# Kernel optimization log

Measured on AMD Instinct MI355X. Metric: run time of the kernel, lower is better.

The kernel has to match this reference:

```python
import jax, jax.numpy as jnp
import numpy as np

EMBED_DIM = 1024
NUM_HEADS = 16
WINDOW = 128  # one-sided window length w; total span 2w+1


def setup_inputs() -> dict:
    key = jax.random.key(0)
    ks = jax.random.split(key, 9)
    D = EMBED_DIM
    x = jax.random.normal(ks[0], (2, 8192, D), dtype=jnp.float32)
    s = 0.02
    Wq = jax.random.normal(ks[1], (D, D), dtype=jnp.float32) * s
    bq = jax.random.normal(ks[2], (D,), dtype=jnp.float32) * s
    Wk = jax.random.normal(ks[3], (D, D), dtype=jnp.float32) * s
    bk = jax.random.normal(ks[4], (D,), dtype=jnp.float32) * s
    Wv = jax.random.normal(ks[5], (D, D), dtype=jnp.float32) * s
    bv = jax.random.normal(ks[6], (D,), dtype=jnp.float32) * s
    Wo = jax.random.normal(ks[7], (D, D), dtype=jnp.float32) * s
    bo = jax.random.normal(ks[8], (D,), dtype=jnp.float32) * s
    return {"x": x, "Wq": Wq, "bq": bq, "Wk": Wk, "bk": bk,
            "Wv": Wv, "bv": bv, "Wo": Wo, "bo": bo}


def _sliding_window_attention(x, Wq, bq, Wk, bk, Wv, bv, Wo, bo):
    B, S, D = x.shape
    H, w = NUM_HEADS, WINDOW
    hd = D // H
    bs = w            # block size = window_length; 3 blocks cover [i-w, i+w]
    nb = S // bs

    def proj(W, b):
        y = x @ W.T + b                              # torch Linear: x @ W.T + b
        return y.reshape(B, S, H, hd).transpose(0, 2, 1, 3)  # [B,H,S,hd]

    q = proj(Wq, bq)
    k = proj(Wk, bk)
    v = proj(Wv, bv)

    qb = q.reshape(B, H, nb, bs, hd)
    # pad K/V with one zero block on each side, then build 3-block contexts
    pad = ((0, 0), (0, 0), (bs, bs), (0, 0))
    kp = jnp.pad(k, pad).reshape(B, H, nb + 2, bs, hd)
    vp = jnp.pad(v, pad).reshape(B, H, nb + 2, bs, hd)
    k_ctx = jnp.concatenate([kp[:, :, :-2], kp[:, :, 1:-1], kp[:, :, 2:]], axis=3)  # [B,H,nb,3bs,hd]
    v_ctx = jnp.concatenate([vp[:, :, :-2], vp[:, :, 1:-1], vp[:, :, 2:]], axis=3)

    scale = 1.0 / np.sqrt(hd).astype(np.float32)
    scores = jnp.einsum('bhnqd,bhnkd->bhnqk', qb, k_ctx) * scale  # [B,H,nb,bs,3bs]

    # band mask: |k_pos - q_pos| <= w, and k_pos in [0, S)
    q_off = jnp.arange(bs)
    k_off = jnp.arange(3 * bs)
    rel = k_off[None, :] - bs - q_off[:, None]                # [bs,3bs]
    win_ok = jnp.abs(rel) <= w
    k_pos = (jnp.arange(nb)[:, None, None] - 1) * bs + k_off[None, None, :]
    valid = (k_pos >= 0) & (k_pos < S)                        # [nb,1,3bs]
    mask = win_ok[None] & valid                               # [nb,bs,3bs]

    scores = jnp.where(mask[None, None], scores, jnp.float32(-jnp.inf))
    weights = jax.nn.softmax(scores, axis=-1)

    out = jnp.einsum('bhnqk,bhnkd->bhnqd', weights, v_ctx)    # [B,H,nb,bs,hd]
    out = out.reshape(B, H, S, hd).transpose(0, 2, 1, 3).reshape(B, S, D)
    return out @ Wo.T + bo


def reference(x, Wq, bq, Wk, bk, Wv, bv, Wo, bo):
    return _sliding_window_attention(x, Wq, bq, Wk, bk, Wv, bv, Wo, bo)
```

## Files before the change

### kernel.cpp

```cpp
#include <hip/hip_runtime.h>

typedef __attribute__((ext_vector_type(4))) float f32x4;
typedef __attribute__((ext_vector_type(8))) short s16x8;

#define MFMA16(a, b, c) __builtin_amdgcn_mfma_f32_16x16x32_bf16((a), (b), (c), 0, 0, 0)

__device__ __forceinline__ unsigned short f2bf_bits(float f) {
  unsigned int u = __float_as_uint(f);
  unsigned int r = (u + 0x7fffu + ((u >> 16) & 1u)) >> 16;
  return (unsigned short)r;
}

__device__ __forceinline__ void gl_lds16(const void* g, void* l) {
  __builtin_amdgcn_global_load_lds((const __attribute__((address_space(1))) void*)g,
                                   (__attribute__((address_space(3))) void*)l, 16, 0, 0);
}

__global__ __launch_bounds__(256) void f2bf_kernel(const float* __restrict__ in,
                                                   unsigned short* __restrict__ out, int n4) {
  int idx = blockIdx.x * 256 + threadIdx.x;
  int stride = gridDim.x * 256;
  for (int i = idx; i < n4; i += stride) {
    float4 v = ((const float4*)in)[i];
    ushort4 o;
    o.x = f2bf_bits(v.x); o.y = f2bf_bits(v.y);
    o.z = f2bf_bits(v.z); o.w = f2bf_bits(v.w);
    ((ushort4*)out)[i] = o;
  }
}

__global__ __launch_bounds__(256) void f2bf_w4(const float* __restrict__ w0,
                                               const float* __restrict__ w1,
                                               const float* __restrict__ w2,
                                               const float* __restrict__ w3,
                                               unsigned short* __restrict__ o0,
                                               unsigned short* __restrict__ o1,
                                               unsigned short* __restrict__ o2,
                                               unsigned short* __restrict__ o3) {
  const int s = blockIdx.y;
  const float* in = (s == 0) ? w0 : (s == 1) ? w1 : (s == 2) ? w2 : w3;
  unsigned short* out = (s == 0) ? o0 : (s == 1) ? o1 : (s == 2) ? o2 : o3;
  int i = blockIdx.x * 256 + threadIdx.x;
  float4 v = ((const float4*)in)[i];
  ushort4 o;
  o.x = f2bf_bits(v.x); o.y = f2bf_bits(v.y);
  o.z = f2bf_bits(v.z); o.w = f2bf_bits(v.w);
  ((ushort4*)out)[i] = o;
}

#define GEMM_CORE64(A_, B_, K_)                                                       \
  f32x4 acc[4][4];                                                                    \
  _Pragma("unroll") for (int i = 0; i < 4; ++i)                                       \
      _Pragma("unroll") for (int j = 0; j < 4; ++j)                                   \
          acc[i][j] = (f32x4){0.f, 0.f, 0.f, 0.f};                                    \
  {                                                                                   \
    const int rb = tid >> 3;                                                          \
    const int cb = (((tid & 7) ^ (rb & 7))) * 8;                                      \
    _Pragma("unroll 1") for (int k0 = 0; k0 < (K_); k0 += 64) {                       \
      _Pragma("unroll") for (int i = 0; i < 4; ++i) {                                 \
        gl_lds16((A_) + (size_t)(rb + 32 * i) * (K_) + k0 + cb, &Al[(tid + 256 * i) * 8]); \
        gl_lds16((B_) + (size_t)(rb + 32 * i) * (K_) + k0 + cb, &Bl[(tid + 256 * i) * 8]); \
      }                                                                               \
      __syncthreads();                                                                \
      _Pragma("unroll") for (int ks = 0; ks < 2; ++ks) {                              \
        s16x8 af[4], bfr[4];                                                          \
        const int pch = ((ks * 4 + quad) ^ (l15 & 7)) * 8;                            \
        _Pragma("unroll") for (int i = 0; i < 4; ++i)                                 \
            af[i] = *(const s16x8*)&Al[(wm + i * 16 + l15) * 64 + pch];               \
        _Pragma("unroll") for (int j = 0; j < 4; ++j)                                 \
            bfr[j] = *(const s16x8*)&Bl[(wn + j * 16 + l15) * 64 + pch];              \
        _Pragma("unroll") for (int i = 0; i < 4; ++i)                                 \
            _Pragma("unroll") for (int j = 0; j < 4; ++j)                             \
                acc[i][j] = MFMA16(af[i], bfr[j], acc[i][j]);                         \
      }                                                                               \
      __syncthreads();                                                                \
    }                                                                                 \
  }

__global__ __launch_bounds__(256) void gemm_qkv(const unsigned short* __restrict__ A,
                                                const unsigned short* __restrict__ Wq,
                                                const unsigned short* __restrict__ Wk,
                                                const unsigned short* __restrict__ Wv,
                                                const float* __restrict__ bq,
                                                const float* __restrict__ bk,
                                                const float* __restrict__ bv,
                                                unsigned short* __restrict__ Qo,
                                                unsigned short* __restrict__ Ko,
                                                unsigned short* __restrict__ Vt) {
  __shared__ unsigned short Al[128 * 64];
  __shared__ unsigned short Bl[128 * 64];
  const int tid = threadIdx.x;
  const int lane = tid & 63, wave = tid >> 6;
  const int l15 = lane & 15, quad = lane >> 4;
  const int wm = (wave >> 1) * 64, wn = (wave & 1) * 64;
  const int bx = blockIdx.x;
  const int sel = blockIdx.y >> 3;
  const int by = blockIdx.y & 7;
  const int K = 1024, N = 1024;

  const unsigned short* W = (sel == 0) ? Wq : (sel == 1) ? Wk : Wv;
  const float* bias = (sel == 0) ? bq : (sel == 1) ? bk : bv;

  const unsigned short* Abase = A + (size_t)bx * 128 * K;
  const unsigned short* Bbase = W + (size_t)by * 128 * K;

  GEMM_CORE64(Abase, Bbase, K)

#pragma unroll
  for (int j = 0; j < 4; ++j) {
    const int cn = by * 128 + wn + j * 16 + l15;
    const float bj = bias[cn];
#pragma unroll
    for (int i = 0; i < 4; ++i) {
      const int r0 = bx * 128 + wm + i * 16 + quad * 4;
#pragma unroll
      for (int r = 0; r < 4; ++r) {
        const int row = r0 + r;
        const float v = acc[i][j][r] + bj;
        if (sel == 0) {
          Qo[(size_t)row * N + cn] = f2bf_bits(v);
        } else if (sel == 1) {
          Ko[(size_t)row * N + cn] = f2bf_bits(v);
        } else {
          Vt[((size_t)(row >> 13) * 1024 + cn) * 8192 + (row & 8191)] = f2bf_bits(v);
        }
      }
    }
  }
}

__global__ __launch_bounds__(256) void gemm_out(const unsigned short* __restrict__ A,
                                                const unsigned short* __restrict__ B,
                                                const float* __restrict__ bias,
                                                float* __restrict__ Cf) {
  __shared__ unsigned short Al[128 * 64];
  __shared__ unsigned short Bl[128 * 64];
  const int tid = threadIdx.x;
  const int lane = tid & 63, wave = tid >> 6;
  const int l15 = lane & 15, quad = lane >> 4;
  const int wm = (wave >> 1) * 64, wn = (wave & 1) * 64;
  const int bx = blockIdx.x, by = blockIdx.y;
  const int K = 1024, N = 1024;

  const unsigned short* Abase = A + (size_t)bx * 128 * K;
  const unsigned short* Bbase = B + (size_t)by * 128 * K;

  GEMM_CORE64(Abase, Bbase, K)

#pragma unroll
  for (int j = 0; j < 4; ++j) {
    const int cn = by * 128 + wn + j * 16 + l15;
    const float bj = bias[cn];
#pragma unroll
    for (int i = 0; i < 4; ++i) {
      const int r0 = bx * 128 + wm + i * 16 + quad * 4;
#pragma unroll
      for (int r = 0; r < 4; ++r) Cf[(size_t)(r0 + r) * N + cn] = acc[i][j][r] + bj;
    }
  }
}

__global__ __launch_bounds__(256, 3) void attn_kernel(const unsigned short* __restrict__ Q,
                                                      const unsigned short* __restrict__ Km,
                                                      const unsigned short* __restrict__ Vt,
                                                      unsigned short* __restrict__ O) {
  const int n = blockIdx.x;
  const int bh = blockIdx.y;
  const int b = bh >> 4, h = bh & 15;
  const int tid = threadIdx.x, lane = tid & 63, wave = tid >> 6;
  const int l15 = lane & 15, quad = lane >> 4;

  __shared__ unsigned short Kl[384 * 64];
  __shared__ unsigned short Ps[4][16 * 40];

  const int base_row = n * 128 - 128;

  for (int i = 0; i < 12; ++i) {
    const int c = i * 256 + tid;
    const int row = c >> 3;
    const int qc = (c & 7) ^ (row & 7);
    int gr = base_row + row;
    gr = min(max(gr, 0), 8191);
    gl_lds16(Km + (size_t)(b * 8192 + gr) * 1024 + h * 64 + qc * 8, &Kl[c * 8]);
  }
  __syncthreads();

  const unsigned short* Vbase = Vt + (size_t)bh * 64 * 8192;
  unsigned short* strip = &Ps[wave][0];

  for (int mt = 0; mt < 2; ++mt) {
    const int qt = wave * 2 + mt;
    const int q0 = n * 128 + qt * 16;
    const int qp = q0 + l15;

    const unsigned short* qptr = Q + (size_t)(b * 8192 + qp) * 1024 + h * 64 + quad * 8;
    const s16x8 bq0 = *(const s16x8*)qptr;
    const s16x8 bq1 = *(const s16x8*)(qptr + 32);

    f32x4 o[4];
#pragma unroll
    for (int dt = 0; dt < 4; ++dt) o[dt] = (f32x4){0.f, 0.f, 0.f, 0.f};
    float lsum = 0.f;

    const int krel0 = qt * 16;

#pragma unroll 1
    for (int p = 0; p < 9; ++p) {
      f32x4 st[2];
#pragma unroll
      for (int tt = 0; tt < 2; ++tt) {
        int rel = krel0 + p * 32 + tt * 16 + l15;
        int rr = min(rel, 383);
        const int ro = rr * 8;
        const int sw = rr & 7;
        const s16x8 ka0 = *(const s16x8*)&Kl[(ro + (quad ^ sw)) * 8];
        const s16x8 ka1 = *(const s16x8*)&Kl[(ro + ((4 + quad) ^ sw)) * 8];
        f32x4 a = (f32x4){0.f, 0.f, 0.f, 0.f};
        a = MFMA16(ka0, bq0, a);
        a = MFMA16(ka1, bq1, a);
        st[tt] = a;
      }
      ushort4 w0, w1;
#pragma unroll
      for (int tt = 0; tt < 2; ++tt) {
        unsigned short* wp = tt ? (unsigned short*)&w1 : (unsigned short*)&w0;
#pragma unroll
        for (int r = 0; r < 4; ++r) {
          const int kp = base_row + krel0 + p * 32 + tt * 16 + quad * 4 + r;
          const int dd = kp - qp;
          const bool ok = (kp >= 0) && (kp < 8192) && (dd >= -128) && (dd <= 128);
          const float pv = ok ? __expf(st[tt][r] * 0.125f) : 0.f;
          lsum += pv;
          wp[r] = f2bf_bits(pv);
        }
      }
      *(ushort4*)&strip[l15 * 40 + quad * 4] = w0;
      *(ushort4*)&strip[l15 * 40 + 16 + quad * 4] = w1;
      const s16x8 pf = *(const s16x8*)&strip[l15 * 40 + quad * 8];
      int kc = base_row + krel0 + p * 32 + quad * 8;
      kc = min(max(kc, 0), 8184);
#pragma unroll
      for (int dt = 0; dt < 4; ++dt) {
        const s16x8 va = *(const s16x8*)(Vbase + (size_t)(dt * 16 + l15) * 8192 + kc);
        o[dt] = MFMA16(va, pf, o[dt]);
      }
    }

    lsum += __shfl_xor(lsum, 16, 64);
    lsum += __shfl_xor(lsum, 32, 64);
    const float rinv = 1.f / lsum;
    unsigned short* obase = O + (size_t)(b * 8192 + qp) * 1024 + h * 64;
#pragma unroll
    for (int dt = 0; dt < 4; ++dt) {
      ushort4 w;
      unsigned short* wp = (unsigned short*)&w;
#pragma unroll
      for (int r = 0; r < 4; ++r) wp[r] = f2bf_bits(o[dt][r] * rinv);
      *(ushort4*)(obase + dt * 16 + quad * 4) = w;
    }
  }
}

extern "C" void kernel_launch(void* const* d_in, const int* in_sizes, int n_in, void* d_out,
                              int out_size, void* d_ws, size_t ws_size, hipStream_t stream) {
  const float* x = (const float*)d_in[0];
  const float* Wq = (const float*)d_in[1];
  const float* bq = (const float*)d_in[2];
  const float* Wk = (const float*)d_in[3];
  const float* bk = (const float*)d_in[4];
  const float* Wv = (const float*)d_in[5];
  const float* bv = (const float*)d_in[6];
  const float* Wo = (const float*)d_in[7];
  const float* bo = (const float*)d_in[8];
  float* out = (float*)d_out;

  const int M = 16384, D = 1024;

  unsigned short* xb = (unsigned short*)d_ws;
  unsigned short* qb = xb + (size_t)M * D;
  unsigned short* kb = qb + (size_t)M * D;
  unsigned short* vt = kb + (size_t)M * D;
  unsigned short* ab = vt + (size_t)M * D;
  unsigned short* wqb = ab + (size_t)M * D;
  unsigned short* wkb = wqb + (size_t)D * D;
  unsigned short* wvb = wkb + (size_t)D * D;
  unsigned short* wob = wvb + (size_t)D * D;

  f2bf_kernel<<<16384, 256, 0, stream>>>(x, xb, M * D / 4);
  f2bf_w4<<<dim3(1024, 4), 256, 0, stream>>>(Wq, Wk, Wv, Wo, wqb, wkb, wvb, wob);

  gemm_qkv<<<dim3(M / 128, 24), 256, 0, stream>>>(xb, wqb, wkb, wvb, bq, bk, bv, qb, kb, vt);

  attn_kernel<<<dim3(64, 32), 256, 0, stream>>>(qb, kb, vt, ab);

  gemm_out<<<dim3(M / 128, D / 128), 256, 0, stream>>>(ab, wob, bo, out);
}
```

Measured before the change: 444.5 us.

## Rewrite projection GEMMs as 256x256 tiles with double-buffered LDS pipeline

Both the QKV and output projection GEMMs move from a 128x128 tile with 4 waves and a single LDS buffer to a 256x256 tile with 8 waves. The new core double-buffers A/B halves in LDS and interleaves global-to-LDS prefetch with MFMA phases, using explicit barriers, waitcnt and setprio. The aim is to raise arithmetic intensity and hide load latency behind the MFMAs. In exchange it uses 64KB of LDS per block, more accumulator registers, fewer blocks per grid, and hand-tuned synchronization that is fragile.

```diff
diff --git a/kernel.cpp b/kernel.cpp
--- a/kernel.cpp
+++ b/kernel.cpp
@@ -48,79 +48,149 @@
   ((ushort4*)out)[i] = o;
 }
 
-#define GEMM_CORE64(A_, B_, K_)                                                       \
-  f32x4 acc[4][4];                                                                    \
-  _Pragma("unroll") for (int i = 0; i < 4; ++i)                                       \
-      _Pragma("unroll") for (int j = 0; j < 4; ++j)                                   \
-          acc[i][j] = (f32x4){0.f, 0.f, 0.f, 0.f};                                    \
-  {                                                                                   \
-    const int rb = tid >> 3;                                                          \
-    const int cb = (((tid & 7) ^ (rb & 7))) * 8;                                      \
-    _Pragma("unroll 1") for (int k0 = 0; k0 < (K_); k0 += 64) {                       \
-      _Pragma("unroll") for (int i = 0; i < 4; ++i) {                                 \
-        gl_lds16((A_) + (size_t)(rb + 32 * i) * (K_) + k0 + cb, &Al[(tid + 256 * i) * 8]); \
-        gl_lds16((B_) + (size_t)(rb + 32 * i) * (K_) + k0 + cb, &Bl[(tid + 256 * i) * 8]); \
-      }                                                                               \
-      __syncthreads();                                                                \
-      _Pragma("unroll") for (int ks = 0; ks < 2; ++ks) {                              \
-        s16x8 af[4], bfr[4];                                                          \
-        const int pch = ((ks * 4 + quad) ^ (l15 & 7)) * 8;                            \
-        _Pragma("unroll") for (int i = 0; i < 4; ++i)                                 \
-            af[i] = *(const s16x8*)&Al[(wm + i * 16 + l15) * 64 + pch];               \
-        _Pragma("unroll") for (int j = 0; j < 4; ++j)                                 \
-            bfr[j] = *(const s16x8*)&Bl[(wn + j * 16 + l15) * 64 + pch];              \
-        _Pragma("unroll") for (int i = 0; i < 4; ++i)                                 \
-            _Pragma("unroll") for (int j = 0; j < 4; ++j)                             \
-                acc[i][j] = MFMA16(af[i], bfr[j], acc[i][j]);                         \
-      }                                                                               \
-      __syncthreads();                                                                \
-    }                                                                                 \
-  }
-
-__global__ __launch_bounds__(256) void gemm_qkv(const unsigned short* __restrict__ A,
-                                                const unsigned short* __restrict__ Wq,
-                                                const unsigned short* __restrict__ Wk,
-                                                const unsigned short* __restrict__ Wv,
-                                                const float* __restrict__ bq,
-                                                const float* __restrict__ bk,
-                                                const float* __restrict__ bv,
-                                                unsigned short* __restrict__ Qo,
-                                                unsigned short* __restrict__ Ko,
-                                                unsigned short* __restrict__ Vt) {
-  __shared__ unsigned short Al[128 * 64];
-  __shared__ unsigned short Bl[128 * 64];
+
+#define S_BARRIER asm volatile("s_barrier" ::: "memory")
+#define WAIT_LGKM0 asm volatile("s_waitcnt lgkmcnt(0)" ::: "memory")
+#define SCHED_FENCE __builtin_amdgcn_sched_barrier(0)
+
+#define STAGE_HALF(gsrc, ldst)                                                   \
+  {                                                                              \
+    _Pragma("unroll") for (int i_ = 0; i_ < 2; ++i_) {                           \
+      const int ci_ = tid + 512 * i_;                                            \
+      const int r_ = ci_ >> 3;                                                   \
+      const int c_ = (ci_ & 7) ^ (r_ & 7);                                       \
+      gl_lds16((gsrc) + (size_t)r_ * 1024 + c_ * 8, (ldst) + ci_ * 8);           \
+    }                                                                            \
+  }
+
+#define LDA8(dst, mf_, ks_)                                                      \
+  dst = *(const s16x8*)&Ahalf[(((mf_) * 16 + l15) * 8 +                          \
+                               (((ks_) * 4 + quad) ^ (l15 & 7))) * 8]
+#define LDB8(dst, nf_, ks_)                                                      \
+  dst = *(const s16x8*)&Bhalf[((bro + (nf_) * 16 + l15) * 8 +                    \
+                               (((ks_) * 4 + quad) ^ (l15 & 7))) * 8]
+
+#define MF_BLOCK(MBASE, NBASE)                                                   \
+  _Pragma("unroll") for (int m_ = 0; m_ < 4; ++m_)                               \
+    _Pragma("unroll") for (int n_ = 0; n_ < 2; ++n_) {                           \
+      acc[(MBASE) + m_][(NBASE) + n_] =                                          \
+          MFMA16(af[m_][0], bf[(NBASE) + n_][0], acc[(MBASE) + m_][(NBASE) + n_]); \
+      acc[(MBASE) + m_][(NBASE) + n_] =                                          \
+          MFMA16(af[m_][1], bf[(NBASE) + n_][1], acc[(MBASE) + m_][(NBASE) + n_]); \
+    }
+
+#define GEMM256_CORE(Ab_, Bb_)                                                   \
+  f32x4 acc[8][4];                                                               \
+  _Pragma("unroll") for (int mi = 0; mi < 8; ++mi)                               \
+      _Pragma("unroll") for (int ni = 0; ni < 4; ++ni)                           \
+          acc[mi][ni] = (f32x4){0.f, 0.f, 0.f, 0.f};                             \
+  {                                                                              \
+    s16x8 af[4][2], bf[4][2];                                                    \
+                 \
+    STAGE_HALF((Ab_), &Al[0][0][0]);                                             \
+    STAGE_HALF((Ab_) + 128 * 1024, &Al[0][1][0]);                                \
+    STAGE_HALF((Bb_), &Bl[0][0][0]);                                             \
+    STAGE_HALF((Bb_) + 128 * 1024, &Bl[0][1][0]);                                \
+    STAGE_HALF((Bb_) + 64, &Bl[1][0][0]);                                        \
+    STAGE_HALF((Bb_) + 128 * 1024 + 64, &Bl[1][1][0]);                           \
+    asm volatile("s_waitcnt vmcnt(4)" ::: "memory");         \
+    S_BARRIER;                                                                   \
+    _Pragma("unroll 2") for (int T = 0; T < 16; ++T) {                           \
+      const int buf_ = T & 1, obuf_ = buf_ ^ 1;                                  \
+      const unsigned short* Ahalf = &Al[buf_][wm][0];                            \
+      const unsigned short* Bhalf = &Bl[buf_][wn >> 1][0];                       \
+          \
+      _Pragma("unroll") for (int m_ = 0; m_ < 4; ++m_) {                         \
+        LDA8(af[m_][0], m_, 0); LDA8(af[m_][1], m_, 1);                          \
+      }                                                                          \
+      _Pragma("unroll") for (int n_ = 0; n_ < 2; ++n_) {                         \
+        LDB8(bf[n_][0], n_, 0); LDB8(bf[n_][1], n_, 1);                          \
+      }                                                                          \
+      if (T < 15) STAGE_HALF((Ab_) + (size_t)(T + 1) * 64, &Al[obuf_][0][0]);    \
+      S_BARRIER; WAIT_LGKM0; SCHED_FENCE;                                        \
+      __builtin_amdgcn_s_setprio(1);                                             \
+      MF_BLOCK(0, 0)                                                             \
+      __builtin_amdgcn_s_setprio(0);                                             \
+      S_BARRIER;                                                                 \
+                   \
+      _Pragma("unroll") for (int n_ = 2; n_ < 4; ++n_) {                         \
+        LDB8(bf[n_][0], n_, 0); LDB8(bf[n_][1], n_, 1);                          \
+      }                                                                          \
+      if (T < 15)                                                                \
+        STAGE_HALF((Ab_) + 128 * 1024 + (size_t)(T + 1) * 64, &Al[obuf_][1][0]); \
+      S_BARRIER; WAIT_LGKM0; SCHED_FENCE;                                        \
+      __builtin_amdgcn_s_setprio(1);                                             \
+      MF_BLOCK(0, 2)                                                             \
+      __builtin_amdgcn_s_setprio(0);                                             \
+      S_BARRIER;                                                                 \
+                   \
+      _Pragma("unroll") for (int m_ = 0; m_ < 4; ++m_) {                         \
+        LDA8(af[m_][0], 4 + m_, 0); LDA8(af[m_][1], 4 + m_, 1);                  \
+      }                                                                          \
+      if (T < 14) STAGE_HALF((Bb_) + (size_t)(T + 2) * 64, &Bl[buf_][0][0]);     \
+      S_BARRIER; WAIT_LGKM0; SCHED_FENCE;                                        \
+      __builtin_amdgcn_s_setprio(1);                                             \
+      MF_BLOCK(4, 0)                                                             \
+      __builtin_amdgcn_s_setprio(0);                                             \
+      S_BARRIER;                                                                 \
+                  \
+      if (T < 14)                                                                \
+        STAGE_HALF((Bb_) + 128 * 1024 + (size_t)(T + 2) * 64, &Bl[buf_][1][0]);  \
+      if (T < 14) {                                                              \
+        asm volatile("s_waitcnt vmcnt(4)" ::: "memory");                         \
+      } else {                                                                   \
+        asm volatile("s_waitcnt vmcnt(0)" ::: "memory");                         \
+      }                                                                          \
+      S_BARRIER; SCHED_FENCE;                                                    \
+      __builtin_amdgcn_s_setprio(1);                                             \
+      MF_BLOCK(4, 2)                                                             \
+      __builtin_amdgcn_s_setprio(0);                                             \
+      S_BARRIER;                                                                 \
+    }                                                                            \
+  }
+
+__global__ __launch_bounds__(512, 2) void gemm_qkv(const unsigned short* __restrict__ A,
+                                                   const unsigned short* __restrict__ Wq,
+                                                   const unsigned short* __restrict__ Wk,
+                                                   const unsigned short* __restrict__ Wv,
+                                                   const float* __restrict__ bq,
+                                                   const float* __restrict__ bk,
+                                                   const float* __restrict__ bv,
+                                                   unsigned short* __restrict__ Qo,
+                                                   unsigned short* __restrict__ Ko,
+                                                   unsigned short* __restrict__ Vt) {
+  __shared__ unsigned short Al[2][2][8192];
+  __shared__ unsigned short Bl[2][2][8192];
   const int tid = threadIdx.x;
   const int lane = tid & 63, wave = tid >> 6;
   const int l15 = lane & 15, quad = lane >> 4;
-  const int wm = (wave >> 1) * 64, wn = (wave & 1) * 64;
+  const int wm = wave >> 2, wn = wave & 3;
+  const int bro = (wn & 1) * 64;
   const int bx = blockIdx.x;
-  const int sel = blockIdx.y >> 3;
-  const int by = blockIdx.y & 7;
-  const int K = 1024, N = 1024;
+  const int sel = blockIdx.y >> 2, byl = blockIdx.y & 3;
 
   const unsigned short* W = (sel == 0) ? Wq : (sel == 1) ? Wk : Wv;
   const float* bias = (sel == 0) ? bq : (sel == 1) ? bk : bv;
-
-  const unsigned short* Abase = A + (size_t)bx * 128 * K;
-  const unsigned short* Bbase = W + (size_t)by * 128 * K;
-
-  GEMM_CORE64(Abase, Bbase, K)
-
-#pragma unroll
-  for (int j = 0; j < 4; ++j) {
-    const int cn = by * 128 + wn + j * 16 + l15;
+  const unsigned short* Ab = A + (size_t)bx * 256 * 1024;
+  const unsigned short* Bb = W + (size_t)byl * 256 * 1024;
+
+  GEMM256_CORE(Ab, Bb)
+
+#pragma unroll
+  for (int nf = 0; nf < 4; ++nf) {
+    const int cn = byl * 256 + wn * 64 + nf * 16 + l15;
     const float bj = bias[cn];
 #pragma unroll
-    for (int i = 0; i < 4; ++i) {
-      const int r0 = bx * 128 + wm + i * 16 + quad * 4;
+    for (int mf = 0; mf < 8; ++mf) {
+      const int r0 = bx * 256 + wm * 128 + mf * 16 + quad * 4;
 #pragma unroll
       for (int r = 0; r < 4; ++r) {
         const int row = r0 + r;
-        const float v = acc[i][j][r] + bj;
+        const float v = acc[mf][nf][r] + bj;
         if (sel == 0) {
-          Qo[(size_t)row * N + cn] = f2bf_bits(v);
+          Qo[(size_t)row * 1024 + cn] = f2bf_bits(v);
         } else if (sel == 1) {
-          Ko[(size_t)row * N + cn] = f2bf_bits(v);
+          Ko[(size_t)row * 1024 + cn] = f2bf_bits(v);
         } else {
           Vt[((size_t)(row >> 13) * 1024 + cn) * 8192 + (row & 8191)] = f2bf_bits(v);
         }
@@ -129,33 +199,33 @@
   }
 }
 
-__global__ __launch_bounds__(256) void gemm_out(const unsigned short* __restrict__ A,
-                                                const unsigned short* __restrict__ B,
-                                                const float* __restrict__ bias,
-                                                float* __restrict__ Cf) {
-  __shared__ unsigned short Al[128 * 64];
-  __shared__ unsigned short Bl[128 * 64];
+__global__ __launch_bounds__(512, 2) void gemm_out(const unsigned short* __restrict__ A,
+                                                   const unsigned short* __restrict__ B,
+                                                   const float* __restrict__ bias,
+                                                   float* __restrict__ Cf) {
+  __shared__ unsigned short Al[2][2][8192];
+  __shared__ unsigned short Bl[2][2][8192];
   const int tid = threadIdx.x;
   const int lane = tid & 63, wave = tid >> 6;
   const int l15 = lane & 15, quad = lane >> 4;
-  const int wm = (wave >> 1) * 64, wn = (wave & 1) * 64;
-  const int bx = blockIdx.x, by = blockIdx.y;
-  const int K = 1024, N = 1024;
-
-  const unsigned short* Abase = A + (size_t)bx * 128 * K;
-  const unsigned short* Bbase = B + (size_t)by * 128 * K;
-
-  GEMM_CORE64(Abase, Bbase, K)
-
-#pragma unroll
-  for (int j = 0; j < 4; ++j) {
-    const int cn = by * 128 + wn + j * 16 + l15;
+  const int wm = wave >> 2, wn = wave & 3;
+  const int bro = (wn & 1) * 64;
+  const int bx = blockIdx.x;
+
+  const unsigned short* Ab = A + (size_t)bx * 256 * 1024;
+  const unsigned short* Bb = B + (size_t)blockIdx.y * 256 * 1024;
+
+  GEMM256_CORE(Ab, Bb)
+
+#pragma unroll
+  for (int nf = 0; nf < 4; ++nf) {
+    const int cn = blockIdx.y * 256 + wn * 64 + nf * 16 + l15;
     const float bj = bias[cn];
 #pragma unroll
-    for (int i = 0; i < 4; ++i) {
-      const int r0 = bx * 128 + wm + i * 16 + quad * 4;
-#pragma unroll
-      for (int r = 0; r < 4; ++r) Cf[(size_t)(r0 + r) * N + cn] = acc[i][j][r] + bj;
+    for (int mf = 0; mf < 8; ++mf) {
+      const int r0 = bx * 256 + wm * 128 + mf * 16 + quad * 4;
+#pragma unroll
+      for (int r = 0; r < 4; ++r) Cf[(size_t)(r0 + r) * 1024 + cn] = acc[mf][nf][r] + bj;
     }
   }
 }
@@ -289,9 +359,9 @@
   f2bf_kernel<<<16384, 256, 0, stream>>>(x, xb, M * D / 4);
   f2bf_w4<<<dim3(1024, 4), 256, 0, stream>>>(Wq, Wk, Wv, Wo, wqb, wkb, wvb, wob);
 
-  gemm_qkv<<<dim3(M / 128, 24), 256, 0, stream>>>(xb, wqb, wkb, wvb, bq, bk, bv, qb, kb, vt);
+  gemm_qkv<<<dim3(M / 256, 12), 512, 0, stream>>>(xb, wqb, wkb, wvb, bq, bk, bv, qb, kb, vt);
 
   attn_kernel<<<dim3(64, 32), 256, 0, stream>>>(qb, kb, vt, ab);
 
-  gemm_out<<<dim3(M / 128, D / 128), 256, 0, stream>>>(ab, wob, bo, out);
-}
+  gemm_out<<<dim3(M / 256, D / 256), 512, 0, stream>>>(ab, wob, bo, out);
+}
```

New measurement: 418.8 us. 5.8% less time.
